# Kernel optimization log

Measured on AMD Instinct MI355X. Metric: run time of the kernel, lower is better.

## Reference

```python
import jax, jax.numpy as jnp
import numpy as np

HEADS = 16
KV_HEADS = 8
HEAD_DIM = 128
ROPE_BASE = 10000.0
RMS_EPS = 1e-5


def rmsnorm(x, w, eps=RMS_EPS):
    x = jnp.clip(x.astype(jnp.float32), -100.0, 100.0)
    var = jnp.clip(jnp.mean(x * x, axis=-1, keepdims=True), eps, None)
    x = x * jax.lax.rsqrt(var + eps)
    x = jnp.clip(x, -10.0, 10.0)
    return w * x


def activation_quant(x):
    x = jnp.clip(x, -50.0, 50.0)
    max_val = jnp.clip(jnp.max(jnp.abs(x), axis=-1, keepdims=True), 0.0001, None)
    scale = 127.0 / max_val
    return jnp.clip(jnp.round(x * scale), -128.0, 127.0) / scale


def weight_quant(w):
    scale = jnp.clip(jnp.mean(jnp.abs(w)), 1e-8, None)
    e = jnp.mean(w)
    return jnp.sign(w - e) * scale


def bitlinear(x, w, norm_w):
    xn = rmsnorm(x, norm_w)
    xq = xn + jax.lax.stop_gradient(activation_quant(xn) - xn)
    wq = w + jax.lax.stop_gradient(weight_quant(w) - w)
    return xq @ wq.T


def rope_tables(seq_len, dim):
    inv_freq = 1.0 / (ROPE_BASE ** (jnp.arange(0, dim, 2, dtype=jnp.float32) / dim))
    freqs = jnp.outer(jnp.arange(seq_len, dtype=jnp.float32), inv_freq)  # [S, dim/2]
    emb = jnp.concatenate([freqs, freqs], axis=-1)  # [S, dim]
    return jnp.cos(emb), jnp.sin(emb)


def rotate_half(x):
    x1, x2 = jnp.split(x, 2, axis=-1)
    return jnp.concatenate([-x2, x1], axis=-1)


def attention_forward(hidden_states, attention_mask, wq, wk, wv, wo, nq, nk, nv, no):
    B, S, H = hidden_states.shape
    q = bitlinear(hidden_states, wq, nq)  # [B,S,nh*hd]
    k = bitlinear(hidden_states, wk, nk)  # [B,S,nkv*hd]
    v = bitlinear(hidden_states, wv, nv)

    q = q.reshape(B, S, HEADS, HEAD_DIM).transpose(0, 2, 1, 3)       # [B,nh,S,hd]
    k = k.reshape(B, S, KV_HEADS, HEAD_DIM).transpose(0, 2, 1, 3)    # [B,nkv,S,hd]
    v = v.reshape(B, S, KV_HEADS, HEAD_DIM).transpose(0, 2, 1, 3)

    cos, sin = rope_tables(S, HEAD_DIM)
    cos = cos[None, None]  # [1,1,S,hd]
    sin = sin[None, None]
    q = q * cos + rotate_half(q) * sin
    k = k * cos + rotate_half(k) * sin

    groups = HEADS // KV_HEADS
    k_exp = jnp.repeat(k, groups, axis=1)  # [B,nh,S,hd]
    v_exp = jnp.repeat(v, groups, axis=1)

    scale = 1.0 / jnp.sqrt(jnp.float32(HEAD_DIM))
    scores = jnp.einsum('bhqd,bhkd->bhqk', q, k_exp) * scale
    scores = scores + attention_mask
    attn = jax.nn.softmax(scores, axis=-1)
    out = jnp.einsum('bhqk,bhkd->bhqd', attn, v_exp)
    out = out.transpose(0, 2, 1, 3).reshape(B, S, HEADS * HEAD_DIM)
    return bitlinear(out, wo, no)


def setup_inputs() -> dict:
    key = jax.random.key(0)
    ks = jax.random.split(key, 6)
    B, S, H = 2, 2048, 2048
    KVH = KV_HEADS * HEAD_DIM
    std = 0.02 / np.sqrt(H)
    return {
        'hidden_states': jax.random.normal(ks[0], (B, S, H), jnp.float32),
        'attention_mask': jnp.zeros((1, 1, S, S), jnp.float32),
        'wq': jax.random.normal(ks[1], (H, H), jnp.float32) * std,
        'wk': jax.random.normal(ks[2], (KVH, H), jnp.float32) * std,
        'wv': jax.random.normal(ks[3], (KVH, H), jnp.float32) * std,
        'wo': jax.random.normal(ks[4], (H, H), jnp.float32) * std,
        'nq': jnp.ones((H,), jnp.float32),
        'nk': jnp.ones((H,), jnp.float32),
        'nv': jnp.ones((H,), jnp.float32),
        'no': jnp.ones((H,), jnp.float32),
    }


def reference(hidden_states, attention_mask, wq, wk, wv, wo, nq, nk, nv, no):
    return attention_forward(hidden_states, attention_mask, wq, wk, wv, wo, nq, nk, nv, no)
```

## Files before the change

kernel.cpp:

```cpp
#include <hip/hip_runtime.h>


#define DI __device__ __forceinline__

using bf16   = __bf16;
using bf16x4 = __attribute__((ext_vector_type(4))) __bf16;
using bf16x8 = __attribute__((ext_vector_type(8))) __bf16;
using f32x4  = __attribute__((ext_vector_type(4))) float;
using i32x4  = __attribute__((ext_vector_type(4))) int;

DI void gl_lds16(void* lds, const void* g) {
  __builtin_amdgcn_global_load_lds((const __attribute__((address_space(1))) void*)g,
                                   (__attribute__((address_space(3))) void*)lds, 16, 0, 0);
}
DI float clampf(float x, float lo, float hi) { return fminf(fmaxf(x, lo), hi); }

template <int N> DI void wait_vm() {
  if constexpr (N == 8)      asm volatile("s_waitcnt vmcnt(8)" ::: "memory");
  else if constexpr (N == 6) asm volatile("s_waitcnt vmcnt(6)" ::: "memory");
  else if constexpr (N == 4) asm volatile("s_waitcnt vmcnt(4)" ::: "memory");
  else                       asm volatile("s_waitcnt vmcnt(0)" ::: "memory");
}

DI float block_sum(float v, float* red, int lane, int w) {
#pragma unroll
  for (int o = 32; o > 0; o >>= 1) v += __shfl_xor(v, o, 64);
  __syncthreads();
  if (lane == 0) red[w] = v;
  __syncthreads();
  return red[0] + red[1] + red[2] + red[3];
}

__global__ void wstats_kernel(const float* wq, const float* wk, const float* wv,
                              const float* wo, float* stats, float* ct, float* st) {
  int t = threadIdx.x;
  int m = blockIdx.y;
  if (m == 4) {
    int idx = blockIdx.x * 256 + t;
#pragma unroll
    for (int k = 0; k < 2; ++k) {
      int e = idx + k * 65536;
      int s = e >> 6, j = e & 63;
      float invf = powf(10000.f, -(float)j * (1.f / 64.f));
      float a = (float)s * invf;
      ct[s * 64 + j] = cosf(a);
      st[s * 64 + j] = sinf(a);
    }
    return;
  }
  __shared__ float red[4], red2[4];
  int lane = t & 63, w = t >> 6;
  const float* src; int n4;
  if (m == 0)      { src = wq; n4 = 1048576; }
  else if (m == 1) { src = wk; n4 = 524288;  }
  else if (m == 2) { src = wv; n4 = 524288;  }
  else             { src = wo; n4 = 1048576; }
  float s = 0.f, sa = 0.f;
  for (int i = blockIdx.x * 256 + t; i < n4; i += 256 * 256) {
    float4 v = ((const float4*)src)[i];
    s  += v.x + v.y + v.z + v.w;
    sa += fabsf(v.x) + fabsf(v.y) + fabsf(v.z) + fabsf(v.w);
  }
#pragma unroll
  for (int o = 32; o > 0; o >>= 1) { s += __shfl_xor(s, o, 64); sa += __shfl_xor(sa, o, 64); }
  if (lane == 0) { red[w] = s; red2[w] = sa; }
  __syncthreads();
  if (t == 0) {
    atomicAdd(&stats[2 * m],     red[0] + red[1] + red[2] + red[3]);
    atomicAdd(&stats[2 * m + 1], red2[0] + red2[1] + red2[2] + red2[3]);
  }
}

__global__ void wsign_kernel(const float* wq, const float* wk, const float* wv, const float* wo,
                             char* sq, char* sk, char* sv, char* so,
                             const float* stats) {
  int m = blockIdx.y;
  const float* src; char* dst; int n4; float cinv;
  if (m == 0)      { src = wq; dst = sq; n4 = 1048576; cinv = 1.f / 4194304.f; }
  else if (m == 1) { src = wk; dst = sk; n4 = 524288;  cinv = 1.f / 2097152.f; }
  else if (m == 2) { src = wv; dst = sv; n4 = 524288;  cinv = 1.f / 2097152.f; }
  else             { src = wo; dst = so; n4 = 1048576; cinv = 1.f / 4194304.f; }
  float e = stats[2 * m] * cinv;
  for (int i = blockIdx.x * 256 + threadIdx.x; i < n4; i += 1024 * 256) {
    float4 v = ((const float4*)src)[i];
    char4 o;
    o.x = v.x > e ? 1 : (v.x < e ? -1 : 0);
    o.y = v.y > e ? 1 : (v.y < e ? -1 : 0);
    o.z = v.z > e ? 1 : (v.z < e ? -1 : 0);
    o.w = v.w > e ? 1 : (v.w < e ? -1 : 0);
    ((char4*)dst)[i] = o;
  }
}

template <int NW>
__launch_bounds__(256)
__global__ void rqnorm_kernel(const float* __restrict__ x,
                              const float* __restrict__ w0, const float* __restrict__ w1,
                              const float* __restrict__ w2,
                              char* a0, char* a1, char* a2,
                              float* r0, float* r1, float* r2) {
  __shared__ float red[4];
  __shared__ float redm[4][NW];
  int t = threadIdx.x, lane = t & 63, w = t >> 6;
  int row = blockIdx.x;
  const float* xr = x + (size_t)row * 2048;
  float4 u0 = ((const float4*)xr)[t * 2], u1 = ((const float4*)xr)[t * 2 + 1];
  float xs[8] = {u0.x, u0.y, u0.z, u0.w, u1.x, u1.y, u1.z, u1.w};
  float ss = 0.f;
#pragma unroll
  for (int e = 0; e < 8; ++e) { xs[e] = clampf(xs[e], -100.f, 100.f); ss += xs[e] * xs[e]; }
  float tot = block_sum(ss, red, lane, w);
  float var = fmaxf(tot * (1.f / 2048.f), 1e-5f);
  float inv = 1.f / sqrtf(var + 1e-5f);
#pragma unroll
  for (int e = 0; e < 8; ++e) xs[e] = clampf(xs[e] * inv, -10.f, 10.f);

  float y[NW][8], am[NW];
#pragma unroll
  for (int m = 0; m < NW; ++m) {
    const float* wt = (m == 0) ? w0 : (m == 1) ? w1 : w2;
    float4 b0 = ((const float4*)wt)[t * 2], b1 = ((const float4*)wt)[t * 2 + 1];
    float wv[8] = {b0.x, b0.y, b0.z, b0.w, b1.x, b1.y, b1.z, b1.w};
    am[m] = 0.f;
#pragma unroll
    for (int e = 0; e < 8; ++e) {
      y[m][e] = clampf(wv[e] * xs[e], -50.f, 50.f);
      am[m] = fmaxf(am[m], fabsf(y[m][e]));
    }
  }
#pragma unroll
  for (int o = 32; o > 0; o >>= 1)
#pragma unroll
    for (int m = 0; m < NW; ++m) am[m] = fmaxf(am[m], __shfl_xor(am[m], o, 64));
  if (lane == 0)
#pragma unroll
    for (int m = 0; m < NW; ++m) redm[w][m] = am[m];
  __syncthreads();
#pragma unroll
  for (int m = 0; m < NW; ++m) {
    char* a = (m == 0) ? a0 : (m == 1) ? a1 : a2;
    float* r = (m == 0) ? r0 : (m == 1) ? r1 : r2;
    float mx = fmaxf(fmaxf(redm[0][m], redm[1][m]), fmaxf(redm[2][m], redm[3][m]));
    float maxval = fmaxf(mx, 1e-4f);
    float sc = 127.f / maxval;
    union { char c[8]; int2 v; } pk;
#pragma unroll
    for (int e = 0; e < 8; ++e)
      pk.c[e] = (char)clampf(rintf(y[m][e] * sc), -128.f, 127.f);
    *(int2*)(a + (size_t)row * 2048 + t * 8) = pk.v;
    if (t == 0) r[row] = maxval * (1.f / 127.f);
  }
}

template <int BM, int BN>
DI void mm_pipe(const char* __restrict__ Ag0, const char* __restrict__ Bg0,
                char* As, char* Bs, int t, i32x4 (&acc)[BM / 64][BN / 32]) {
  constexpr int MR = BM / 64, NR = BN / 32;
  constexpr int AL = BM / 64, BL = BN / 64;
  constexpr int NT = 16;
  int lane = t & 63, l15 = lane & 15, quad = lane >> 4;
  int wv = t >> 6, wm = wv >> 1, wn = wv & 1;
  const char* agp[AL]; const char* bgp[BL];
#pragma unroll
  for (int i = 0; i < AL; ++i) {
    int c = t + i * 512, row = c >> 3, cr = c & 7;
    agp[i] = Ag0 + (size_t)row * 2048 + (cr ^ (row & 7)) * 16;
  }
#pragma unroll
  for (int i = 0; i < BL; ++i) {
    int c = t + i * 512, row = c >> 3, cr = c & 7;
    bgp[i] = Bg0 + (size_t)row * 2048 + (cr ^ (row & 7)) * 16;
  }
  auto stage = [&](int buf, int kt) {
    int kb = kt * 128;
#pragma unroll
    for (int i = 0; i < AL; ++i)
      gl_lds16(As + buf * (BM * 128) + (t + i * 512) * 16, agp[i] + kb);
#pragma unroll
    for (int i = 0; i < BL; ++i)
      gl_lds16(Bs + buf * (BN * 128) + (t + i * 512) * 16, bgp[i] + kb);
  };
  stage(0, 0);
  stage(1, 1);
  int arow = wm * (BM / 4) + l15;
  int brow = wn * (BN / 2) + l15;
  int sa = arow & 7, sb = brow & 7;
  for (int kt = 0; kt < NT; ++kt) {
    int cur = kt & 1;
    if (kt == NT - 1) wait_vm<0>(); else wait_vm<AL + BL>();
    __builtin_amdgcn_sched_barrier(0);
    __builtin_amdgcn_s_barrier();
    __builtin_amdgcn_sched_barrier(0);
    const char* Ac = As + cur * (BM * 128);
    const char* Bc = Bs + cur * (BN * 128);
    __builtin_amdgcn_s_setprio(1);
#pragma unroll
    for (int ks = 0; ks < 2; ++ks) {
      int aco = ((ks * 4 + quad) ^ sa) * 16;
      int bco = ((ks * 4 + quad) ^ sb) * 16;
      i32x4 af[MR], bfr[NR];
#pragma unroll
      for (int m = 0; m < MR; ++m)
        af[m] = *(const i32x4*)(Ac + (arow + m * 16) * 128 + aco);
#pragma unroll
      for (int n = 0; n < NR; ++n)
        bfr[n] = *(const i32x4*)(Bc + (brow + n * 16) * 128 + bco);
#pragma unroll
      for (int m = 0; m < MR; ++m)
#pragma unroll
        for (int n = 0; n < NR; ++n)
          acc[m][n] = __builtin_amdgcn_mfma_i32_16x16x64_i8(af[m], bfr[n], acc[m][n], 0, 0, 0);
    }
    __builtin_amdgcn_s_setprio(0);
    __builtin_amdgcn_sched_barrier(0);
    __builtin_amdgcn_s_barrier();
    __builtin_amdgcn_sched_barrier(0);
    if (kt + 2 < NT) stage(cur, kt + 2);
  }
}

__launch_bounds__(512, 2)
__global__ void qkv_gemm(const char* __restrict__ Aq, const char* __restrict__ Ak,
                         const char* __restrict__ Av, const char* __restrict__ Ball,
                         const float* __restrict__ rq, const float* __restrict__ rk,
                         const float* __restrict__ rv, const float* __restrict__ stats,
                         bf16* __restrict__ qr, bf16* __restrict__ kr,
                         bf16* __restrict__ vt,
                         const float* __restrict__ ct, const float* __restrict__ st) {
  __shared__ char As[2 * 256 * 128];
  __shared__ char Bs[2 * 256 * 128];
  int t = threadIdx.x;
  int bid = blockIdx.x;
  int swz = (bid & 7) * 32 + (bid >> 3);
  int x = swz >> 4, mt = swz & 15;
  int m0 = mt * 256;
  const char* A; const float* rs; float sw;
  if (x < 8)       { A = Aq; rs = rq; sw = stats[1] * (1.f / 4194304.f); }
  else if (x < 12) { A = Ak; rs = rk; sw = stats[3] * (1.f / 2097152.f); }
  else             { A = Av; rs = rv; sw = stats[5] * (1.f / 2097152.f); }
  sw = fmaxf(sw, 1e-8f);
  i32x4 acc[4][8] = {};
  mm_pipe<256, 256>(A + (size_t)m0 * 2048, Ball + (size_t)(x * 256) * 2048, As, Bs, t, acc);

  int lane = t & 63, l15 = lane & 15, quad = lane >> 4;
  int wv = t >> 6, wm = wv >> 1, wn = wv & 1;
  if (x < 12) {
    constexpr float QROPE = 0.08838834764831845f * 1.4426950408889634f;
    float qmul = (x < 8) ? QROPE : 1.f;
    bf16* outb = (x < 8) ? qr : kr;
    int h = (x < 8) ? (x * 2 + wn) : ((x - 8) * 2 + wn);
    int nh = (x < 8) ? 16 : 8;
#pragma unroll
    for (int m = 0; m < 4; ++m)
#pragma unroll
      for (int r = 0; r < 4; ++r) {
        int row = m0 + wm * 64 + m * 16 + quad * 4 + r;
        float rsc = rs[row] * sw * qmul;
        int s = row & 2047, b = row >> 11;
        size_t base = ((size_t)(b * nh + h) * 2048 + s) * 128;
#pragma unroll
        for (int n = 0; n < 4; ++n) {
          int d = n * 16 + l15;
          float x1 = (float)acc[m][n][r] * rsc;
          float x2 = (float)acc[m][n + 4][r] * rsc;
          float c = ct[s * 64 + d], sn = st[s * 64 + d];
          outb[base + d]      = (bf16)(x1 * c - x2 * sn);
          outb[base + d + 64] = (bf16)(x2 * c + x1 * sn);
        }
      }
  } else {
    int n0g = (x - 12) * 256 + wn * 128;
    int kvh = n0g >> 7;
    int btok = m0 >> 11;
    int s0 = (m0 & 2047) + wm * 64 + quad * 4;
#pragma unroll
    for (int m = 0; m < 4; ++m)
#pragma unroll
      for (int n = 0; n < 8; ++n) {
        int d = n * 16 + l15;
        bf16x4 pk;
#pragma unroll
        for (int r = 0; r < 4; ++r) {
          int row = m0 + wm * 64 + m * 16 + quad * 4 + r;
          pk[r] = (bf16)((float)acc[m][n][r] * (rs[row] * sw));
        }
        *(bf16x4*)(vt + ((size_t)(btok * 8 + kvh) * 128 + d) * 2048 + s0 + m * 16) = pk;
      }
  }
}

__launch_bounds__(512, 2)
__global__ void gemm_o(const char* __restrict__ A, const char* __restrict__ Bw,
                       const float* __restrict__ rs, const float* __restrict__ stats,
                       float* __restrict__ out) {
  __shared__ char As[2 * 128 * 128];
  __shared__ char Bs[2 * 256 * 128];
  int t = threadIdx.x;
  int bid = blockIdx.x;
  int swz = (bid & 7) * 32 + (bid >> 3);
  int x = swz & 7, mt = swz >> 3;
  int m0 = mt * 128, n0 = x * 256;
  i32x4 acc[2][8] = {};
  mm_pipe<128, 256>(A + (size_t)m0 * 2048, Bw + (size_t)n0 * 2048, As, Bs, t, acc);
  float sw = fmaxf(stats[7] * (1.f / 4194304.f), 1e-8f);
  int lane = t & 63, l15 = lane & 15, quad = lane >> 4;
  int wv = t >> 6, wm = wv >> 1, wn = wv & 1;
#pragma unroll
  for (int m = 0; m < 2; ++m)
#pragma unroll
    for (int r = 0; r < 4; ++r) {
      int row = m0 + wm * 32 + m * 16 + quad * 4 + r;
      float rsc = rs[row] * sw;
#pragma unroll
      for (int n = 0; n < 8; ++n)
        out[(size_t)row * 2048 + n0 + wn * 128 + n * 16 + l15] = (float)acc[m][n][r] * rsc;
    }
}

__launch_bounds__(512, 4)
__global__ void attn_kernel(const bf16* __restrict__ Q, const bf16* __restrict__ Kc,
                            const bf16* __restrict__ Vt, const float* __restrict__ mask,
                            float* __restrict__ Oout) {
  constexpr float L2E  = 1.4426950408889634f;
  constexpr float DTHR = 8.f * L2E;
  __shared__ bf16 Ks[2][64 * 128];
  __shared__ bf16 Vs[2][128 * 64];
  __shared__ bf16 Ps[128 * 64];
  int t = threadIdx.x, w = t >> 6, lane = t & 63;
  int l15 = lane & 15, quad = lane >> 4;
  int bh = blockIdx.y, b = bh >> 4, h = bh & 15, kvh = h >> 1;
  int q0 = blockIdx.x * 128;
  const bf16* Qb = Q + (size_t)(b * 16 + h) * 2048 * 128;
  const bf16* Kb = Kc + (size_t)(b * 8 + kvh) * 2048 * 128;
  const bf16* Vb = Vt + (size_t)(b * 8 + kvh) * 128 * 2048;

  int qloc = w * 16 + l15;
  int qg = q0 + qloc;

  bf16x8 qf[4];
#pragma unroll
  for (int kc = 0; kc < 4; ++kc)
    qf[kc] = *(const bf16x8*)(Qb + (size_t)qg * 128 + kc * 32 + quad * 8);

  f32x4 Oa[8] = {};
  float mrow = -1e30f, lrow = 0.f;

  auto stage = [&](int buf, int kt) {
    int kk0 = kt * 64;
#pragma unroll
    for (int i = 0; i < 2; ++i) {
      int c = t + i * 512;
      int kr = c >> 4, c16 = c & 15;
      gl_lds16(&Ks[buf][c * 8],
               Kb + (size_t)(kk0 + kr) * 128 + ((c16 ^ (kr & 15)) * 8));
    }
#pragma unroll
    for (int i = 0; i < 2; ++i) {
      int c = t + i * 512;
      int vr = c >> 3, c8 = c & 7;
      gl_lds16(&Vs[buf][c * 8],
               Vb + (size_t)vr * 2048 + kk0 + ((c8 ^ (vr & 7)) * 8));
    }
  };

  stage(0, 0);

  f32x4 mv[4];
#pragma unroll
  for (int k2 = 0; k2 < 4; ++k2)
    mv[k2] = *(const f32x4*)(mask + (size_t)qg * 2048 + k2 * 16 + quad * 4);

  for (int kt = 0; kt < 32; ++kt) {
    int cur = kt & 1;
    __syncthreads();
    if (kt < 31) stage(cur ^ 1, kt + 1);

    f32x4 Sacc[4] = {};
    __builtin_amdgcn_s_setprio(1);
#pragma unroll
    for (int kc = 0; kc < 4; ++kc) {
      bf16x8 kf[4];
#pragma unroll
      for (int k2 = 0; k2 < 4; ++k2)
        kf[k2] = *(const bf16x8*)(&Ks[cur][(k2 * 16 + l15) * 128 + (((kc * 4 + quad) ^ l15) * 8)]);
#pragma unroll
      for (int k2 = 0; k2 < 4; ++k2)
        Sacc[k2] = __builtin_amdgcn_mfma_f32_16x16x32_bf16(kf[k2], qf[kc], Sacc[k2], 0, 0, 0);
    }
    __builtin_amdgcn_s_setprio(0);

#pragma unroll
    for (int k2 = 0; k2 < 4; ++k2)
#pragma unroll
      for (int r = 0; r < 4; ++r)
        Sacc[k2][r] = fmaf(mv[k2][r], L2E, Sacc[k2][r]);
    f32x4 vm;
#pragma unroll
    for (int r = 0; r < 4; ++r)
      vm[r] = fmaxf(fmaxf(Sacc[0][r], Sacc[1][r]), fmaxf(Sacc[2][r], Sacc[3][r]));
    float mx = fmaxf(fmaxf(vm[0], vm[1]), fmaxf(vm[2], vm[3]));
    mx = fmaxf(mx, __shfl_xor(mx, 16, 64));
    mx = fmaxf(mx, __shfl_xor(mx, 32, 64));
    if (!__all(mx <= mrow + DTHR)) {
      float mnew = fmaxf(mrow, mx);
      float alpha = exp2f(mrow - mnew);
      mrow = mnew;
      lrow *= alpha;
#pragma unroll
      for (int dt = 0; dt < 8; ++dt) Oa[dt] *= alpha;
    }
    f32x4 vs = {0.f, 0.f, 0.f, 0.f};
#pragma unroll
    for (int k2 = 0; k2 < 4; ++k2) {
      bf16x4 pk;
#pragma unroll
      for (int r = 0; r < 4; ++r) {
        float p = exp2f(Sacc[k2][r] - mrow);
        vs[r] += p;
        pk[r] = (bf16)p;
      }
      int c = k2 * 2 + (quad >> 1);
      *(bf16x4*)(&Ps[qloc * 64 + ((c ^ (qloc & 7)) * 8) + (quad & 1) * 4]) = pk;
    }
    float rsum = (vs[0] + vs[1]) + (vs[2] + vs[3]);
    rsum += __shfl_xor(rsum, 16, 64);
    rsum += __shfl_xor(rsum, 32, 64);
    lrow += rsum;

    if (kt < 31) {
      int kk1 = (kt + 1) * 64;
#pragma unroll
      for (int k2 = 0; k2 < 4; ++k2)
        mv[k2] = *(const f32x4*)(mask + (size_t)qg * 2048 + kk1 + k2 * 16 + quad * 4);
    }

    __builtin_amdgcn_s_setprio(1);
#pragma unroll
    for (int kc = 0; kc < 2; ++kc) {
      bf16x8 pf = *(const bf16x8*)(&Ps[qloc * 64 + (((kc * 4 + quad) ^ (l15 & 7)) * 8)]);
#pragma unroll
      for (int dt = 0; dt < 8; ++dt) {
        bf16x8 vf = *(const bf16x8*)(&Vs[cur][(dt * 16 + l15) * 64 +
                                              (((kc * 4 + quad) ^ (l15 & 7)) * 8)]);
        Oa[dt] = __builtin_amdgcn_mfma_f32_16x16x32_bf16(vf, pf, Oa[dt], 0, 0, 0);
      }
    }
    __builtin_amdgcn_s_setprio(0);
  }

  float inv = 1.f / lrow;
  int token = b * 2048 + qg;
#pragma unroll
  for (int dt = 0; dt < 8; ++dt) {
    f32x4 o = Oa[dt] * inv;
    *(f32x4*)(Oout + (size_t)token * 2048 + h * 128 + dt * 16 + quad * 4) = o;
  }
}

extern "C" void kernel_launch(void* const* d_in, const int* in_sizes, int n_in,
                              void* d_out, int out_size, void* d_ws, size_t ws_size,
                              hipStream_t stream) {
  const float* hidden = (const float*)d_in[0];
  const float* mask   = (const float*)d_in[1];
  const float* wq = (const float*)d_in[2];
  const float* wk = (const float*)d_in[3];
  const float* wv = (const float*)d_in[4];
  const float* wo = (const float*)d_in[5];
  const float* nq = (const float*)d_in[6];
  const float* nk = (const float*)d_in[7];
  const float* nv = (const float*)d_in[8];
  const float* no = (const float*)d_in[9];
  float* out = (float*)d_out;
  char* ws = (char*)d_ws;

  constexpr size_t O_STATS = 0;
  constexpr size_t O_CT    = 256;
  constexpr size_t O_ST    = O_CT  + 524288;
  constexpr size_t O_SQ    = O_ST  + 524288;
  constexpr size_t O_SK    = O_SQ  + 4194304;
  constexpr size_t O_SV    = O_SK  + 2097152;
  constexpr size_t O_SO    = O_SV  + 2097152;
  constexpr size_t O_RSQ   = O_SO  + 4194304;
  constexpr size_t O_RSK   = O_RSQ + 16384;
  constexpr size_t O_RSV   = O_RSK + 16384;
  constexpr size_t O_RSO   = O_RSV + 16384;
  constexpr size_t O_AQQ   = O_RSO + 16384;
  constexpr size_t O_AQK   = O_AQQ + 8388608;
  constexpr size_t O_AQV   = O_AQK + 8388608;
  constexpr size_t O_QR    = O_AQV + 8388608;
  constexpr size_t O_KR    = O_QR  + 16777216;
  constexpr size_t O_VT    = O_KR  + 8388608;
  constexpr size_t O_ATTN  = O_VT  + 8388608;
  constexpr size_t O_AQO   = O_AQQ;

  float* stats = (float*)(ws + O_STATS);
  float* ct = (float*)(ws + O_CT);
  float* st = (float*)(ws + O_ST);

  (void)hipMemsetAsync(ws + O_STATS, 0, 256, stream);

  wstats_kernel<<<dim3(256, 5), 256, 0, stream>>>(wq, wk, wv, wo, stats, ct, st);
  wsign_kernel<<<dim3(1024, 4), 256, 0, stream>>>(wq, wk, wv, wo,
      ws + O_SQ, ws + O_SK, ws + O_SV, ws + O_SO, stats);

  rqnorm_kernel<3><<<dim3(4096), 256, 0, stream>>>(hidden, nq, nk, nv,
      ws + O_AQQ, ws + O_AQK, ws + O_AQV,
      (float*)(ws + O_RSQ), (float*)(ws + O_RSK), (float*)(ws + O_RSV));

  qkv_gemm<<<dim3(256), 512, 0, stream>>>(
      ws + O_AQQ, ws + O_AQK, ws + O_AQV, ws + O_SQ,
      (const float*)(ws + O_RSQ), (const float*)(ws + O_RSK), (const float*)(ws + O_RSV),
      stats, (bf16*)(ws + O_QR), (bf16*)(ws + O_KR), (bf16*)(ws + O_VT), ct, st);

  attn_kernel<<<dim3(16, 32), 512, 0, stream>>>(
      (const bf16*)(ws + O_QR), (const bf16*)(ws + O_KR), (const bf16*)(ws + O_VT),
      mask, (float*)(ws + O_ATTN));

  rqnorm_kernel<1><<<dim3(4096), 256, 0, stream>>>((const float*)(ws + O_ATTN), no, no, no,
      ws + O_AQO, ws + O_AQO, ws + O_AQO,
      (float*)(ws + O_RSO), (float*)(ws + O_RSO), (float*)(ws + O_RSO));

  gemm_o<<<dim3(256), 512, 0, stream>>>(
      ws + O_AQO, ws + O_SO, (float*)(ws + O_RSO), stats, out);

  (void)in_sizes; (void)n_in; (void)out_size; (void)ws_size;
}
```

Measured before the change: 367.6 us.

## Software-pipeline QK^T one tile ahead of softmax/PV in attention kernel

Restructures the flash-attention main loop so the QK^T MFMA for tile kt+1 is issued before the softmax and PV of tile kt, using ping-pong score accumulators. K and V staging are split, with K prefetched two tiles ahead. Explicit vmcnt waits and barriers replace the single syncthreads. The aim is to overlap the exp/softmax VALU work with matrix-core work and hide load latency. In exchange it uses more registers and depends on fragile hand-written wait counts, which could lower occupancy or cause races.

Result: slower. 452.5 us (+23.1%).

```diff
diff --git a/kernel.cpp b/kernel.cpp
--- a/kernel.cpp
+++ b/kernel.cpp
@@ -344,60 +344,79 @@
 
   f32x4 Oa[8] = {};
   float mrow = -1e30f, lrow = 0.f;
-
-  auto stage = [&](int buf, int kt) {
+  f32x4 mv[4];
+
+  auto stageK = [&](int buf, int kt) {
     int kk0 = kt * 64;
 #pragma unroll
     for (int i = 0; i < 2; ++i) {
-      int c = t + i * 512;
-      int kr = c >> 4, c16 = c & 15;
-      gl_lds16(&Ks[buf][c * 8],
-               Kb + (size_t)(kk0 + kr) * 128 + ((c16 ^ (kr & 15)) * 8));
-    }
+      int c = t + i * 512, kr = c >> 4, c16 = c & 15;
+      gl_lds16(&Ks[buf][c * 8], Kb + (size_t)(kk0 + kr) * 128 + ((c16 ^ (kr & 15)) * 8));
+    }
+  };
+  auto stageV = [&](int buf, int kt) {
+    int kk0 = kt * 64;
 #pragma unroll
     for (int i = 0; i < 2; ++i) {
-      int c = t + i * 512;
-      int vr = c >> 3, c8 = c & 7;
-      gl_lds16(&Vs[buf][c * 8],
-               Vb + (size_t)vr * 2048 + kk0 + ((c8 ^ (vr & 7)) * 8));
+      int c = t + i * 512, vr = c >> 3, c8 = c & 7;
+      gl_lds16(&Vs[buf][c * 8], Vb + (size_t)vr * 2048 + kk0 + ((c8 ^ (vr & 7)) * 8));
     }
   };
-
-  stage(0, 0);
-
-  f32x4 mv[4];
-#pragma unroll
-  for (int k2 = 0; k2 < 4; ++k2)
-    mv[k2] = *(const f32x4*)(mask + (size_t)qg * 2048 + k2 * 16 + quad * 4);
-
-  for (int kt = 0; kt < 32; ++kt) {
-    int cur = kt & 1;
-    __syncthreads();
-    if (kt < 31) stage(cur ^ 1, kt + 1);
-
-    f32x4 Sacc[4] = {};
+  auto loadmask = [&](int kt) {
+    int kk = kt * 64;
+#pragma unroll
+    for (int k2 = 0; k2 < 4; ++k2)
+      mv[k2] = *(const f32x4*)(mask + (size_t)qg * 2048 + kk + k2 * 16 + quad * 4);
+  };
+  auto qkt = [&](int buf, f32x4 (&S)[4]) {
     __builtin_amdgcn_s_setprio(1);
 #pragma unroll
     for (int kc = 0; kc < 4; ++kc) {
       bf16x8 kf[4];
 #pragma unroll
       for (int k2 = 0; k2 < 4; ++k2)
-        kf[k2] = *(const bf16x8*)(&Ks[cur][(k2 * 16 + l15) * 128 + (((kc * 4 + quad) ^ l15) * 8)]);
+        kf[k2] = *(const bf16x8*)(&Ks[buf][(k2 * 16 + l15) * 128 + (((kc * 4 + quad) ^ l15) * 8)]);
 #pragma unroll
       for (int k2 = 0; k2 < 4; ++k2)
-        Sacc[k2] = __builtin_amdgcn_mfma_f32_16x16x32_bf16(kf[k2], qf[kc], Sacc[k2], 0, 0, 0);
+        S[k2] = __builtin_amdgcn_mfma_f32_16x16x32_bf16(kf[k2], qf[kc], S[k2], 0, 0, 0);
     }
     __builtin_amdgcn_s_setprio(0);
-
+  };
+
+  stageK(0, 0);
+  stageV(0, 0);
+  stageK(1, 1);
+  loadmask(0);
+  asm volatile("s_waitcnt vmcnt(8)" ::: "memory");
+  __builtin_amdgcn_sched_barrier(0);
+  __builtin_amdgcn_s_barrier();
+  __builtin_amdgcn_sched_barrier(0);
+  f32x4 SA[4] = {}, SB[4] = {};
+  qkt(0, SA);
+
+  auto iter = [&](int kt, f32x4 (&Sin)[4], f32x4 (&Sout)[4]) {
+    int cur = kt & 1;
+    asm volatile("s_waitcnt vmcnt(4)" ::: "memory");
+    __builtin_amdgcn_sched_barrier(0);
+    __builtin_amdgcn_s_barrier();
+    __builtin_amdgcn_sched_barrier(0);
+    if (kt < 31) stageV(cur ^ 1, kt + 1);
+    if (kt < 30) stageK(cur, kt + 2);
+    __builtin_amdgcn_sched_barrier(0);
+    if (kt < 31) {
+#pragma unroll
+      for (int k2 = 0; k2 < 4; ++k2) Sout[k2] = f32x4{0.f, 0.f, 0.f, 0.f};
+      qkt(cur ^ 1, Sout);
+    }
 #pragma unroll
     for (int k2 = 0; k2 < 4; ++k2)
 #pragma unroll
       for (int r = 0; r < 4; ++r)
-        Sacc[k2][r] = fmaf(mv[k2][r], L2E, Sacc[k2][r]);
+        Sin[k2][r] = fmaf(mv[k2][r], L2E, Sin[k2][r]);
     f32x4 vm;
 #pragma unroll
     for (int r = 0; r < 4; ++r)
-      vm[r] = fmaxf(fmaxf(Sacc[0][r], Sacc[1][r]), fmaxf(Sacc[2][r], Sacc[3][r]));
+      vm[r] = fmaxf(fmaxf(Sin[0][r], Sin[1][r]), fmaxf(Sin[2][r], Sin[3][r]));
     float mx = fmaxf(fmaxf(vm[0], vm[1]), fmaxf(vm[2], vm[3]));
     mx = fmaxf(mx, __shfl_xor(mx, 16, 64));
     mx = fmaxf(mx, __shfl_xor(mx, 32, 64));
@@ -415,7 +434,7 @@
       bf16x4 pk;
 #pragma unroll
       for (int r = 0; r < 4; ++r) {
-        float p = exp2f(Sacc[k2][r] - mrow);
+        float p = exp2f(Sin[k2][r] - mrow);
         vs[r] += p;
         pk[r] = (bf16)p;
       }
@@ -427,12 +446,7 @@
     rsum += __shfl_xor(rsum, 32, 64);
     lrow += rsum;
 
-    if (kt < 31) {
-      int kk1 = (kt + 1) * 64;
-#pragma unroll
-      for (int k2 = 0; k2 < 4; ++k2)
-        mv[k2] = *(const f32x4*)(mask + (size_t)qg * 2048 + kk1 + k2 * 16 + quad * 4);
-    }
+    if (kt < 31) loadmask(kt + 1);
 
     __builtin_amdgcn_s_setprio(1);
 #pragma unroll
@@ -446,6 +460,11 @@
       }
     }
     __builtin_amdgcn_s_setprio(0);
+  };
+
+  for (int kt2 = 0; kt2 < 16; ++kt2) {
+    iter(2 * kt2,     SA, SB);
+    iter(2 * kt2 + 1, SB, SA);
   }
 
   float inv = 1.f / lrow;
```

## Fuse weight sign and QKV norm kernels; keep P in registers for PV MFMA

Applied to the files above, without the earlier changes.

Merges the weight-sign kernel and the QKV rmsnorm/quantize kernel into one launch, with extra blocks handling weight binarization, which removes a launch and lets the two run concurrently. In attention, the softmax probabilities stay in registers and feed 16x16x16 bf16 MFMAs directly instead of being written to and read back from LDS. This drops the P shared buffer and its LDS traffic, but uses twice as many smaller MFMA instructions and narrower V loads from LDS.

Measured after the change: 367.0 us. Within noise of the previous version (-0.2%).

```diff
diff --git a/kernel.cpp b/kernel.cpp
--- a/kernel.cpp
+++ b/kernel.cpp
@@ -14,6 +14,11 @@
                                    (__attribute__((address_space(3))) void*)lds, 16, 0, 0);
 }
 DI float clampf(float x, float lo, float hi) { return fminf(fmaxf(x, lo), hi); }
+
+DI void mfma16(f32x4& acc, bf16x4 a, bf16x4 b) {
+  asm("v_mfma_f32_16x16x16_bf16 %0, %1, %2, %0"
+      : "+v"(acc) : "v"(a), "v"(b));
+}
 
 template <int N> DI void wait_vm() {
   if constexpr (N == 8)      asm volatile("s_waitcnt vmcnt(8)" ::: "memory");
@@ -71,24 +76,87 @@
   }
 }
 
-__global__ void wsign_kernel(const float* wq, const float* wk, const float* wv, const float* wo,
-                             char* sq, char* sk, char* sv, char* so,
-                             const float* stats) {
-  int m = blockIdx.y;
-  const float* src; char* dst; int n4; float cinv;
-  if (m == 0)      { src = wq; dst = sq; n4 = 1048576; cinv = 1.f / 4194304.f; }
-  else if (m == 1) { src = wk; dst = sk; n4 = 524288;  cinv = 1.f / 2097152.f; }
-  else if (m == 2) { src = wv; dst = sv; n4 = 524288;  cinv = 1.f / 2097152.f; }
-  else             { src = wo; dst = so; n4 = 1048576; cinv = 1.f / 4194304.f; }
-  float e = stats[2 * m] * cinv;
-  for (int i = blockIdx.x * 256 + threadIdx.x; i < n4; i += 1024 * 256) {
-    float4 v = ((const float4*)src)[i];
-    char4 o;
-    o.x = v.x > e ? 1 : (v.x < e ? -1 : 0);
-    o.y = v.y > e ? 1 : (v.y < e ? -1 : 0);
-    o.z = v.z > e ? 1 : (v.z < e ? -1 : 0);
-    o.w = v.w > e ? 1 : (v.w < e ? -1 : 0);
-    ((char4*)dst)[i] = o;
+__launch_bounds__(256)
+__global__ void prep_kernel(const float* __restrict__ x,
+                            const float* __restrict__ w0, const float* __restrict__ w1,
+                            const float* __restrict__ w2,
+                            char* a0, char* a1, char* a2,
+                            float* r0, float* r1, float* r2,
+                            const float* wq, const float* wk, const float* wv,
+                            const float* wo,
+                            char* sq, char* sk, char* sv, char* so,
+                            const float* __restrict__ stats) {
+  int t = threadIdx.x;
+  if (blockIdx.x >= 4096) {
+    int bid = blockIdx.x - 4096;
+    int m = bid >> 10;
+    const float* src; char* dst; int n4; float cinv;
+    if (m == 0)      { src = wq; dst = sq; n4 = 1048576; cinv = 1.f / 4194304.f; }
+    else if (m == 1) { src = wk; dst = sk; n4 = 524288;  cinv = 1.f / 2097152.f; }
+    else if (m == 2) { src = wv; dst = sv; n4 = 524288;  cinv = 1.f / 2097152.f; }
+    else             { src = wo; dst = so; n4 = 1048576; cinv = 1.f / 4194304.f; }
+    float e = stats[2 * m] * cinv;
+    for (int i = (bid & 1023) * 256 + t; i < n4; i += 1024 * 256) {
+      float4 v = ((const float4*)src)[i];
+      char4 o;
+      o.x = v.x > e ? 1 : (v.x < e ? -1 : 0);
+      o.y = v.y > e ? 1 : (v.y < e ? -1 : 0);
+      o.z = v.z > e ? 1 : (v.z < e ? -1 : 0);
+      o.w = v.w > e ? 1 : (v.w < e ? -1 : 0);
+      ((char4*)dst)[i] = o;
+    }
+    return;
+  }
+  __shared__ float red[4];
+  __shared__ float redm[4][3];
+  int lane = t & 63, w = t >> 6;
+  int row = blockIdx.x;
+  const float* xr = x + (size_t)row * 2048;
+  float4 u0 = ((const float4*)xr)[t * 2], u1 = ((const float4*)xr)[t * 2 + 1];
+  float xs[8] = {u0.x, u0.y, u0.z, u0.w, u1.x, u1.y, u1.z, u1.w};
+  float ss = 0.f;
+#pragma unroll
+  for (int e = 0; e < 8; ++e) { xs[e] = clampf(xs[e], -100.f, 100.f); ss += xs[e] * xs[e]; }
+  float tot = block_sum(ss, red, lane, w);
+  float var = fmaxf(tot * (1.f / 2048.f), 1e-5f);
+  float inv = 1.f / sqrtf(var + 1e-5f);
+#pragma unroll
+  for (int e = 0; e < 8; ++e) xs[e] = clampf(xs[e] * inv, -10.f, 10.f);
+
+  float y[3][8], am[3];
+#pragma unroll
+  for (int m = 0; m < 3; ++m) {
+    const float* wt = (m == 0) ? w0 : (m == 1) ? w1 : w2;
+    float4 b0 = ((const float4*)wt)[t * 2], b1 = ((const float4*)wt)[t * 2 + 1];
+    float wv8[8] = {b0.x, b0.y, b0.z, b0.w, b1.x, b1.y, b1.z, b1.w};
+    am[m] = 0.f;
+#pragma unroll
+    for (int e = 0; e < 8; ++e) {
+      y[m][e] = clampf(wv8[e] * xs[e], -50.f, 50.f);
+      am[m] = fmaxf(am[m], fabsf(y[m][e]));
+    }
+  }
+#pragma unroll
+  for (int o = 32; o > 0; o >>= 1)
+#pragma unroll
+    for (int m = 0; m < 3; ++m) am[m] = fmaxf(am[m], __shfl_xor(am[m], o, 64));
+  if (lane == 0)
+#pragma unroll
+    for (int m = 0; m < 3; ++m) redm[w][m] = am[m];
+  __syncthreads();
+#pragma unroll
+  for (int m = 0; m < 3; ++m) {
+    char* a = (m == 0) ? a0 : (m == 1) ? a1 : a2;
+    float* r = (m == 0) ? r0 : (m == 1) ? r1 : r2;
+    float mx = fmaxf(fmaxf(redm[0][m], redm[1][m]), fmaxf(redm[2][m], redm[3][m]));
+    float maxval = fmaxf(mx, 1e-4f);
+    float sc = 127.f / maxval;
+    union { char c[8]; int2 v; } pk;
+#pragma unroll
+    for (int e = 0; e < 8; ++e)
+      pk.c[e] = (char)clampf(rintf(y[m][e] * sc), -128.f, 127.f);
+    *(int2*)(a + (size_t)row * 2048 + t * 8) = pk.v;
+    if (t == 0) r[row] = maxval * (1.f / 127.f);
   }
 }
 
@@ -120,11 +188,11 @@
   for (int m = 0; m < NW; ++m) {
     const float* wt = (m == 0) ? w0 : (m == 1) ? w1 : w2;
     float4 b0 = ((const float4*)wt)[t * 2], b1 = ((const float4*)wt)[t * 2 + 1];
-    float wv[8] = {b0.x, b0.y, b0.z, b0.w, b1.x, b1.y, b1.z, b1.w};
+    float wv8[8] = {b0.x, b0.y, b0.z, b0.w, b1.x, b1.y, b1.z, b1.w};
     am[m] = 0.f;
 #pragma unroll
     for (int e = 0; e < 8; ++e) {
-      y[m][e] = clampf(wv[e] * xs[e], -50.f, 50.f);
+      y[m][e] = clampf(wv8[e] * xs[e], -50.f, 50.f);
       am[m] = fmaxf(am[m], fabsf(y[m][e]));
     }
   }
@@ -325,7 +393,6 @@
   constexpr float DTHR = 8.f * L2E;
   __shared__ bf16 Ks[2][64 * 128];
   __shared__ bf16 Vs[2][128 * 64];
-  __shared__ bf16 Ps[128 * 64];
   int t = threadIdx.x, w = t >> 6, lane = t & 63;
   int l15 = lane & 15, quad = lane >> 4;
   int bh = blockIdx.y, b = bh >> 4, h = bh & 15, kvh = h >> 1;
@@ -409,18 +476,16 @@
 #pragma unroll
       for (int dt = 0; dt < 8; ++dt) Oa[dt] *= alpha;
     }
+    bf16x4 pkv[4];
     f32x4 vs = {0.f, 0.f, 0.f, 0.f};
 #pragma unroll
     for (int k2 = 0; k2 < 4; ++k2) {
-      bf16x4 pk;
 #pragma unroll
       for (int r = 0; r < 4; ++r) {
         float p = exp2f(Sacc[k2][r] - mrow);
         vs[r] += p;
-        pk[r] = (bf16)p;
+        pkv[k2][r] = (bf16)p;
       }
-      int c = k2 * 2 + (quad >> 1);
-      *(bf16x4*)(&Ps[qloc * 64 + ((c ^ (qloc & 7)) * 8) + (quad & 1) * 4]) = pk;
     }
     float rsum = (vs[0] + vs[1]) + (vs[2] + vs[3]);
     rsum += __shfl_xor(rsum, 16, 64);
@@ -436,13 +501,14 @@
 
     __builtin_amdgcn_s_setprio(1);
 #pragma unroll
-    for (int kc = 0; kc < 2; ++kc) {
-      bf16x8 pf = *(const bf16x8*)(&Ps[qloc * 64 + (((kc * 4 + quad) ^ (l15 & 7)) * 8)]);
+    for (int k2 = 0; k2 < 4; ++k2) {
+      int chnk_base = k2 * 2 + (quad >> 1);
+      int hoff = (quad & 1) * 4;
 #pragma unroll
       for (int dt = 0; dt < 8; ++dt) {
-        bf16x8 vf = *(const bf16x8*)(&Vs[cur][(dt * 16 + l15) * 64 +
-                                              (((kc * 4 + quad) ^ (l15 & 7)) * 8)]);
-        Oa[dt] = __builtin_amdgcn_mfma_f32_16x16x32_bf16(vf, pf, Oa[dt], 0, 0, 0);
+        int row = dt * 16 + l15;
+        bf16x4 vf = *(const bf16x4*)(&Vs[cur][row * 64 + ((chnk_base ^ (row & 7)) * 8) + hoff]);
+        mfma16(Oa[dt], vf, pkv[k2]);
       }
     }
     __builtin_amdgcn_s_setprio(0);
@@ -500,12 +566,12 @@
   (void)hipMemsetAsync(ws + O_STATS, 0, 256, stream);
 
   wstats_kernel<<<dim3(256, 5), 256, 0, stream>>>(wq, wk, wv, wo, stats, ct, st);
-  wsign_kernel<<<dim3(1024, 4), 256, 0, stream>>>(wq, wk, wv, wo,
+
+  prep_kernel<<<dim3(8192), 256, 0, stream>>>(hidden, nq, nk, nv,
+      ws + O_AQQ, ws + O_AQK, ws + O_AQV,
+      (float*)(ws + O_RSQ), (float*)(ws + O_RSK), (float*)(ws + O_RSV),
+      wq, wk, wv, wo,
       ws + O_SQ, ws + O_SK, ws + O_SV, ws + O_SO, stats);
-
-  rqnorm_kernel<3><<<dim3(4096), 256, 0, stream>>>(hidden, nq, nk, nv,
-      ws + O_AQQ, ws + O_AQK, ws + O_AQV,
-      (float*)(ws + O_RSQ), (float*)(ws + O_RSK), (float*)(ws + O_RSV));
 
   qkv_gemm<<<dim3(256), 512, 0, stream>>>(
       ws + O_AQQ, ws + O_AQK, ws + O_AQV, ws + O_SQ,
```
